# Optimization experiments

Measured on AMD Instinct MI355X. Metric: run time of the kernel, lower is better.

Reference implementation:

```python
import jax, jax.numpy as jnp
import numpy as np

P_IN = 32  # MODEL_CONFIG['p_in']; note: all 32 sample points share the same offsets in the source


def _bilinear_border(feat, sx, sy):
    """Replicates F.grid_sample(mode='bilinear', padding_mode='border', align_corners=False)
    for a single point per (b, n). feat: [B,C,H,W]; sx, sy: [B,N] in pixel coords.
    align_corners=False unnormalization of grid built as 2*s/size - 1 gives px = s - 0.5.
    Returns [B,N,C]."""
    H, W = feat.shape[-2], feat.shape[-1]
    px = jnp.clip(sx - 0.5, 0.0, W - 1.0)  # border padding clamps coords
    py = jnp.clip(sy - 0.5, 0.0, H - 1.0)
    x0 = jnp.floor(px)
    y0 = jnp.floor(py)
    wx = (px - x0)[..., None]  # [B,N,1]
    wy = (py - y0)[..., None]
    x0i = x0.astype(jnp.int32)
    y0i = y0.astype(jnp.int32)
    x1i = jnp.minimum(x0i + 1, W - 1)
    y1i = jnp.minimum(y0i + 1, H - 1)

    def gather(f, yi, xi):  # f [C,H,W], yi/xi [N] -> [N,C]
        return f[:, yi, xi].T

    g = jax.vmap(gather)  # over batch
    v00 = g(feat, y0i, x0i)
    v01 = g(feat, y0i, x1i)
    v10 = g(feat, y1i, x0i)
    v11 = g(feat, y1i, x1i)
    return (v00 * (1 - wx) * (1 - wy) + v01 * wx * (1 - wy)
            + v10 * (1 - wx) * wy + v11 * wx * wy)


def _forward(feats, query_pos, query_content, W_off, b_off, sigma_z):
    offsets = query_content @ W_off + b_off  # [B,N,3]
    x, y, z, r = (query_pos[..., i] for i in range(4))
    dx, dy, dz = offsets[..., 0], offsets[..., 1], offsets[..., 2]
    sx = x + dx * (2.0 ** (z - r))
    sy = y + dy * (2.0 ** (z + r))
    sz = z + dz
    L = len(feats)
    levels = jnp.arange(L, dtype=sz.dtype)
    # gaussian z weight, then softmax over levels (as in source: softmax of the exp values)
    w = jnp.exp(-((sz[..., None] - levels) ** 2) / (2.0 * sigma_z ** 2))  # [B,N,L]
    zw = jax.nn.softmax(w, axis=-1)
    out = sum(zw[..., l:l + 1] * _bilinear_border(feats[l], sx, sy) for l in range(L))  # [B,N,C]
    B, N, C = out.shape
    # all P_IN sample points use identical coords in the source -> broadcast
    return jnp.broadcast_to(out[:, :, None, :], (B, N, P_IN, C))


def setup_inputs() -> dict:
    key = jax.random.key(0)
    ks = jax.random.split(key, 8)
    B, N, C = 8, 300, 256
    sizes = [(100, 100), (50, 50), (25, 25), (13, 13)]
    feats = [jax.random.normal(ks[i], (B, C, h, w), dtype=jnp.float32)
             for i, (h, w) in enumerate(sizes)]
    u = jax.random.uniform(ks[4], (B, N, 4), dtype=jnp.float32)
    # x in [0,100), y in [0,100) (level-0 pixel coords), z in [0,4), r in [0,1)
    query_pos = u * jnp.array([100.0, 100.0, 4.0, 1.0], dtype=jnp.float32)
    query_content = jax.random.normal(ks[5], (B, N, C), dtype=jnp.float32)
    W_off = jax.random.normal(ks[6], (C, 3), dtype=jnp.float32) * 0.02
    b_off = jnp.zeros((3,), dtype=jnp.float32)
    sigma_z = jnp.ones((1,), dtype=jnp.float32) * 0.5
    return {"feat0": feats[0], "feat1": feats[1], "feat2": feats[2], "feat3": feats[3],
            "query_pos": query_pos, "query_content": query_content,
            "W_off": W_off, "b_off": b_off, "sigma_z": sigma_z}


def reference(feat0, feat1, feat2, feat3, query_pos, query_content, W_off, b_off, sigma_z):
    return _forward([feat0, feat1, feat2, feat3], query_pos, query_content, W_off, b_off, sigma_z)
```

## Files before the change

kernel.cpp:

```cpp
#include <hip/hip_runtime.h>

constexpr int Bc = 8;
constexpr int Nc = 300;
constexpr int Cc = 256;
constexpr int Pc = 32;

typedef float f32x4 __attribute__((ext_vector_type(4)));

constexpr int L1_OFF = 0;
constexpr int L2_OFF = 2500;
constexpr int L3_OFF = 3125;
constexpr int STAGE_FLOATS = 3296;

__device__ __forceinline__ void gl_lds16(const void* g, void* l) {
    __builtin_amdgcn_global_load_lds(
        (const __attribute__((address_space(1))) void*)g,
        (__attribute__((address_space(3))) void*)l, 16, 0, 0);
}
__device__ __forceinline__ void gl_lds4(const void* g, void* l) {
    __builtin_amdgcn_global_load_lds(
        (const __attribute__((address_space(1))) void*)g,
        (__attribute__((address_space(3))) void*)l, 4, 0, 0);
}

__global__ __launch_bounds__(256) void params_kernel(
    const float* __restrict__ qpos, const float* __restrict__ qcont,
    const float* __restrict__ Woff, const float* __restrict__ boff,
    const float* __restrict__ sigma, float* __restrict__ params)
{
    const int w = threadIdx.x >> 6;
    const int lane = threadIdx.x & 63;
    const int q = blockIdx.x * 4 + w;

    f32x4 qc = *(const f32x4*)&qcont[(size_t)q * Cc + lane * 4];
    float p0 = 0.f, p1 = 0.f, p2 = 0.f;
#pragma unroll
    for (int j = 0; j < 4; ++j) {
        const float* wr = &Woff[(lane * 4 + j) * 3];
        p0 += qc[j] * wr[0];
        p1 += qc[j] * wr[1];
        p2 += qc[j] * wr[2];
    }
#pragma unroll
    for (int off = 32; off > 0; off >>= 1) {
        p0 += __shfl_down(p0, off, 64);
        p1 += __shfl_down(p1, off, 64);
        p2 += __shfl_down(p2, off, 64);
    }
    if (lane == 0) {
        float dx = p0 + boff[0];
        float dy = p1 + boff[1];
        float dz = p2 + boff[2];
        float x = qpos[q * 4 + 0];
        float y = qpos[q * 4 + 1];
        float z = qpos[q * 4 + 2];
        float r = qpos[q * 4 + 3];
        float sx = x + dx * exp2f(z - r);
        float sy = y + dy * exp2f(z + r);
        float sz = z + dz;
        float sg = sigma[0];
        float inv = 1.0f / (2.0f * sg * sg);
        float e[4];
        float s = 0.f;
#pragma unroll
        for (int l = 0; l < 4; ++l) {
            float d = sz - (float)l;
            float wgt = __expf(-d * d * inv);
            e[l] = __expf(wgt);
            s += e[l];
        }
        float rs = 1.0f / s;
        params[q * 8 + 0] = sx;
        params[q * 8 + 1] = sy;
#pragma unroll
        for (int l = 0; l < 4; ++l) params[q * 8 + 2 + l] = e[l] * rs;
    }
}

struct BilinW { int i00, i01, i10, i11; float wx, wy; };
__device__ __forceinline__ BilinW bilin(int W, float sx, float sy) {
    float px = fminf(fmaxf(sx - 0.5f, 0.f), (float)(W - 1));
    float py = fminf(fmaxf(sy - 0.5f, 0.f), (float)(W - 1));
    float x0f = floorf(px);
    float y0f = floorf(py);
    int x0 = (int)x0f;
    int y0 = (int)y0f;
    int x1 = min(x0 + 1, W - 1);
    int y1 = min(y0 + 1, W - 1);
    BilinW r;
    r.wx = px - x0f;
    r.wy = py - y0f;
    r.i00 = y0 * W + x0; r.i01 = y0 * W + x1;
    r.i10 = y1 * W + x0; r.i11 = y1 * W + x1;
    return r;
}
__device__ __forceinline__ float blend(float v00, float v01, float v10, float v11,
                                       float wx, float wy) {
    float top = v00 + wx * (v01 - v00);
    float bot = v10 + wx * (v11 - v10);
    return top + wy * (bot - top);
}

__global__ __launch_bounds__(256, 8) void sample_kernel(
    const float* __restrict__ f0, const float* __restrict__ f1,
    const float* __restrict__ f2, const float* __restrict__ f3,
    const float* __restrict__ params, float* __restrict__ outT)
{
    __shared__ __align__(16) float sl[STAGE_FLOATS];
    const int bc = blockIdx.x;
    const int t = threadIdx.x;
    const int b = bc >> 8;
    const int wave = t >> 6;
    const int lane = t & 63;

    const int q0 = b * Nc + t;
    const bool has2 = (t < Nc - 256);
    f32x4 pa0 = *(const f32x4*)&params[(size_t)q0 * 8];
    f32x4 pb0 = *(const f32x4*)&params[(size_t)q0 * 8 + 4];
    f32x4 pa1 = {0, 0, 0, 0}, pb1 = {0, 0, 0, 0};
    if (has2) {
        pa1 = *(const f32x4*)&params[(size_t)(q0 + 256) * 8];
        pb1 = *(const f32x4*)&params[(size_t)(q0 + 256) * 8 + 4];
    }
    const float sx0 = pa0.x, sy0 = pa0.y;
    const float sx1 = pa1.x, sy1 = pa1.y;

    {
        const char* g1 = (const char*)(f1 + (size_t)bc * 2500);
        char* l1 = (char*)&sl[L1_OFF];
        for (int i = wave; i < 9; i += 4)
            gl_lds16(g1 + i * 1024 + lane * 16, l1 + i * 1024);
        if (wave == 2 && lane < 49)
            gl_lds16(g1 + 9 * 1024 + lane * 16, l1 + 9 * 1024);
        const char* g2 = (const char*)(f2 + (size_t)bc * 625);
        char* l2 = (char*)&sl[L2_OFF];
        for (int i = wave; i < 9; i += 4)
            gl_lds4(g2 + i * 256 + lane * 4, l2 + i * 256);
        if (wave == 1 && lane < 49)
            gl_lds4(g2 + 9 * 256 + lane * 4, l2 + 9 * 256);
        const char* g3 = (const char*)(f3 + (size_t)bc * 169);
        char* l3 = (char*)&sl[L3_OFF];
        for (int i = wave; i < 2; i += 4)
            gl_lds4(g3 + i * 256 + lane * 4, l3 + i * 256);
        if (wave == 3 && lane < 41)
            gl_lds4(g3 + 2 * 256 + lane * 4, l3 + 2 * 256);
    }

    const float* base0 = f0 + (size_t)bc * 10000;
    const BilinW w00 = bilin(100, sx0, sy0);
    float a00 = base0[w00.i00];
    float a01 = base0[w00.i01];
    float a10 = base0[w00.i10];
    float a11 = base0[w00.i11];
    BilinW w01;
    float b00 = 0.f, b01 = 0.f, b10 = 0.f, b11 = 0.f;
    if (has2) {
        w01 = bilin(100, sx1, sy1);
        b00 = base0[w01.i00];
        b01 = base0[w01.i01];
        b10 = base0[w01.i10];
        b11 = base0[w01.i11];
    }

    __syncthreads();

    {
        BilinW w1 = bilin(50, sx0, sy0);
        BilinW w2 = bilin(25, sx0, sy0);
        BilinW w3 = bilin(13, sx0, sy0);
        float acc = pa0.z * blend(a00, a01, a10, a11, w00.wx, w00.wy)
                  + pa0.w * blend(sl[L1_OFF + w1.i00], sl[L1_OFF + w1.i01],
                                  sl[L1_OFF + w1.i10], sl[L1_OFF + w1.i11], w1.wx, w1.wy)
                  + pb0.x * blend(sl[L2_OFF + w2.i00], sl[L2_OFF + w2.i01],
                                  sl[L2_OFF + w2.i10], sl[L2_OFF + w2.i11], w2.wx, w2.wy)
                  + pb0.y * blend(sl[L3_OFF + w3.i00], sl[L3_OFF + w3.i01],
                                  sl[L3_OFF + w3.i10], sl[L3_OFF + w3.i11], w3.wx, w3.wy);
        outT[(size_t)bc * Nc + t] = acc;
    }
    if (has2) {
        BilinW w1 = bilin(50, sx1, sy1);
        BilinW w2 = bilin(25, sx1, sy1);
        BilinW w3 = bilin(13, sx1, sy1);
        float acc = pa1.z * blend(b00, b01, b10, b11, w01.wx, w01.wy)
                  + pa1.w * blend(sl[L1_OFF + w1.i00], sl[L1_OFF + w1.i01],
                                  sl[L1_OFF + w1.i10], sl[L1_OFF + w1.i11], w1.wx, w1.wy)
                  + pb1.x * blend(sl[L2_OFF + w2.i00], sl[L2_OFF + w2.i01],
                                  sl[L2_OFF + w2.i10], sl[L2_OFF + w2.i11], w2.wx, w2.wy)
                  + pb1.y * blend(sl[L3_OFF + w3.i00], sl[L3_OFF + w3.i01],
                                  sl[L3_OFF + w3.i10], sl[L3_OFF + w3.i11], w3.wx, w3.wy);
        outT[(size_t)bc * Nc + t + 256] = acc;
    }
}

__global__ __launch_bounds__(256) void broadcast_kernel(
    const float* __restrict__ outT, float* __restrict__ out)
{
    __shared__ float sval[Cc];
    const int q = blockIdx.x;
    const int b = q / Nc;
    const int n = q - b * Nc;
    const int c = threadIdx.x;
    sval[c] = outT[((size_t)(b * Cc + c)) * Nc + n];
    __syncthreads();

    const int wave = threadIdx.x >> 6;
    const int c4 = (threadIdx.x & 63) * 4;
    f32x4 val = *(const f32x4*)&sval[c4];
    float* obase = out + (size_t)q * (Pc * Cc) + c4;
#pragma unroll
    for (int p = wave; p < Pc; p += 4) {
        __builtin_nontemporal_store(val, (f32x4*)(obase + p * Cc));
    }
}

__global__ __launch_bounds__(256) void sampling3d_fallback(
    const float* __restrict__ f0, const float* __restrict__ f1,
    const float* __restrict__ f2, const float* __restrict__ f3,
    const float* __restrict__ qpos, const float* __restrict__ qcont,
    const float* __restrict__ Woff, const float* __restrict__ boff,
    const float* __restrict__ sigma, float* __restrict__ out)
{
    const int q = blockIdx.x;
    const int b = q / Nc;
    const int c = threadIdx.x;
    float qc = qcont[q * Cc + c];
    float p0 = qc * Woff[c * 3 + 0];
    float p1 = qc * Woff[c * 3 + 1];
    float p2 = qc * Woff[c * 3 + 2];
#pragma unroll
    for (int off = 32; off > 0; off >>= 1) {
        p0 += __shfl_down(p0, off, 64);
        p1 += __shfl_down(p1, off, 64);
        p2 += __shfl_down(p2, off, 64);
    }
    __shared__ float red[4][3];
    __shared__ float par[8];
    __shared__ float accs[Cc];
    const int wave = threadIdx.x >> 6;
    if ((threadIdx.x & 63) == 0) { red[wave][0] = p0; red[wave][1] = p1; red[wave][2] = p2; }
    __syncthreads();
    if (threadIdx.x == 0) {
        float dx = red[0][0] + red[1][0] + red[2][0] + red[3][0] + boff[0];
        float dy = red[0][1] + red[1][1] + red[2][1] + red[3][1] + boff[1];
        float dz = red[0][2] + red[1][2] + red[2][2] + red[3][2] + boff[2];
        float x = qpos[q * 4 + 0], y = qpos[q * 4 + 1];
        float z = qpos[q * 4 + 2], r = qpos[q * 4 + 3];
        float sx = x + dx * exp2f(z - r);
        float sy = y + dy * exp2f(z + r);
        float sz = z + dz;
        float sg = sigma[0];
        float inv = 1.0f / (2.0f * sg * sg);
        float e[4]; float s = 0.f;
#pragma unroll
        for (int l = 0; l < 4; ++l) {
            float d = sz - (float)l;
            float w = __expf(-d * d * inv);
            e[l] = __expf(w);
            s += e[l];
        }
        float rs = 1.0f / s;
        par[0] = sx; par[1] = sy;
#pragma unroll
        for (int l = 0; l < 4; ++l) par[2 + l] = e[l] * rs;
    }
    __syncthreads();
    const float sx = par[0];
    const float sy = par[1];
    const float* const fs[4] = {f0, f1, f2, f3};
    const int HWs[4] = {100, 50, 25, 13};
    float acc = 0.f;
#pragma unroll
    for (int l = 0; l < 4; ++l) {
        const int W = HWs[l];
        float px = fminf(fmaxf(sx - 0.5f, 0.f), (float)(W - 1));
        float py = fminf(fmaxf(sy - 0.5f, 0.f), (float)(W - 1));
        float x0f = floorf(px), y0f = floorf(py);
        float wx = px - x0f, wy = py - y0f;
        int x0 = (int)x0f, y0 = (int)y0f;
        int x1 = min(x0 + 1, W - 1), y1 = min(y0 + 1, W - 1);
        const float* base = fs[l] + (size_t)((b * Cc + c) * W) * W;
        float v00 = base[y0 * W + x0];
        float v01 = base[y0 * W + x1];
        float v10 = base[y1 * W + x0];
        float v11 = base[y1 * W + x1];
        float top = v00 + wx * (v01 - v00);
        float bot = v10 + wx * (v11 - v10);
        acc += par[2 + l] * (top + wy * (bot - top));
    }
    accs[c] = acc;
    __syncthreads();
    const int c4 = (threadIdx.x & 63) * 4;
    f32x4 val = *(const f32x4*)&accs[c4];
    float* obase = out + (size_t)q * (Pc * Cc) + c4;
#pragma unroll
    for (int p = wave; p < Pc; p += 4) {
        __builtin_nontemporal_store(val, (f32x4*)(obase + p * Cc));
    }
}

extern "C" void kernel_launch(void* const* d_in, const int* in_sizes, int n_in,
                              void* d_out, int out_size, void* d_ws, size_t ws_size,
                              hipStream_t stream) {
    const float* f0    = (const float*)d_in[0];
    const float* f1    = (const float*)d_in[1];
    const float* f2    = (const float*)d_in[2];
    const float* f3    = (const float*)d_in[3];
    const float* qpos  = (const float*)d_in[4];
    const float* qcont = (const float*)d_in[5];
    const float* Woff  = (const float*)d_in[6];
    const float* boff  = (const float*)d_in[7];
    const float* sigma = (const float*)d_in[8];
    float* out = (float*)d_out;

    const size_t params_bytes = (size_t)Bc * Nc * 8 * sizeof(float);
    const size_t outT_bytes   = (size_t)Bc * Cc * Nc * sizeof(float);

    if (ws_size >= params_bytes + outT_bytes) {
        float* params = (float*)d_ws;
        float* outT   = (float*)((char*)d_ws + params_bytes);
        params_kernel<<<Bc * Nc / 4, 256, 0, stream>>>(qpos, qcont, Woff, boff, sigma, params);
        sample_kernel<<<Bc * Cc, 256, 0, stream>>>(f0, f1, f2, f3, params, outT);
        broadcast_kernel<<<Bc * Nc, 256, 0, stream>>>(outT, out);
    } else {
        sampling3d_fallback<<<Bc * Nc, 256, 0, stream>>>(
            f0, f1, f2, f3, qpos, qcont, Woff, boff, sigma, out);
    }
}
```

Before: 187.3 us.

## Stage level-0 feature map in LDS and broadcast four queries per block

The sample kernel now copies the whole 100x100 level-0 channel plane into shared memory with async global-to-LDS loads, replacing scattered per-thread global gathers. LDS use rises to about 53 KB per block, so occupancy is lowered to 3 blocks, and the kernel reads all 40 KB of f0 per channel instead of only the touched pixels. The broadcast kernel now handles four queries per block, using one vector load from outT per thread, and launches a quarter as many blocks.

New measurement: 189.5 us. Within noise of the previous version (+1.2%).

```diff
diff --git a/kernel.cpp b/kernel.cpp
--- a/kernel.cpp
+++ b/kernel.cpp
@@ -7,10 +7,11 @@
 
 typedef float f32x4 __attribute__((ext_vector_type(4)));
 
-constexpr int L1_OFF = 0;
-constexpr int L2_OFF = 2500;
-constexpr int L3_OFF = 3125;
-constexpr int STAGE_FLOATS = 3296;
+constexpr int F0_OFF = 0;
+constexpr int S1_OFF = 10000;
+constexpr int S2_OFF = 12500;
+constexpr int S3_OFF = 13125;
+constexpr int STAGE2_FLOATS = 13296;
 
 __device__ __forceinline__ void gl_lds16(const void* g, void* l) {
     __builtin_amdgcn_global_load_lds(
@@ -101,12 +102,12 @@
     return top + wy * (bot - top);
 }
 
-__global__ __launch_bounds__(256, 8) void sample_kernel(
+__global__ __launch_bounds__(256, 3) void sample_kernel(
     const float* __restrict__ f0, const float* __restrict__ f1,
     const float* __restrict__ f2, const float* __restrict__ f3,
     const float* __restrict__ params, float* __restrict__ outT)
 {
-    __shared__ __align__(16) float sl[STAGE_FLOATS];
+    __shared__ __align__(16) float sl[STAGE2_FLOATS];
     const int bc = blockIdx.x;
     const int t = threadIdx.x;
     const int b = bc >> 8;
@@ -126,68 +127,62 @@
     const float sx1 = pa1.x, sy1 = pa1.y;
 
     {
+        const char* g0 = (const char*)(f0 + (size_t)bc * 10000);
+        char* l0 = (char*)&sl[F0_OFF];
+        for (int i = wave; i < 39; i += 4)
+            gl_lds16(g0 + i * 1024 + lane * 16, l0 + i * 1024);
+        if (wave == 0 && lane < 4)
+            gl_lds16(g0 + 39 * 1024 + lane * 16, l0 + 39 * 1024);
         const char* g1 = (const char*)(f1 + (size_t)bc * 2500);
-        char* l1 = (char*)&sl[L1_OFF];
+        char* l1 = (char*)&sl[S1_OFF];
         for (int i = wave; i < 9; i += 4)
             gl_lds16(g1 + i * 1024 + lane * 16, l1 + i * 1024);
-        if (wave == 2 && lane < 49)
+        if (wave == 1 && lane < 49)
             gl_lds16(g1 + 9 * 1024 + lane * 16, l1 + 9 * 1024);
         const char* g2 = (const char*)(f2 + (size_t)bc * 625);
-        char* l2 = (char*)&sl[L2_OFF];
+        char* l2 = (char*)&sl[S2_OFF];
         for (int i = wave; i < 9; i += 4)
             gl_lds4(g2 + i * 256 + lane * 4, l2 + i * 256);
-        if (wave == 1 && lane < 49)
+        if (wave == 2 && lane < 49)
             gl_lds4(g2 + 9 * 256 + lane * 4, l2 + 9 * 256);
         const char* g3 = (const char*)(f3 + (size_t)bc * 169);
-        char* l3 = (char*)&sl[L3_OFF];
+        char* l3 = (char*)&sl[S3_OFF];
         for (int i = wave; i < 2; i += 4)
             gl_lds4(g3 + i * 256 + lane * 4, l3 + i * 256);
         if (wave == 3 && lane < 41)
             gl_lds4(g3 + 2 * 256 + lane * 4, l3 + 2 * 256);
     }
 
-    const float* base0 = f0 + (size_t)bc * 10000;
-    const BilinW w00 = bilin(100, sx0, sy0);
-    float a00 = base0[w00.i00];
-    float a01 = base0[w00.i01];
-    float a10 = base0[w00.i10];
-    float a11 = base0[w00.i11];
-    BilinW w01;
-    float b00 = 0.f, b01 = 0.f, b10 = 0.f, b11 = 0.f;
-    if (has2) {
-        w01 = bilin(100, sx1, sy1);
-        b00 = base0[w01.i00];
-        b01 = base0[w01.i01];
-        b10 = base0[w01.i10];
-        b11 = base0[w01.i11];
-    }
-
     __syncthreads();
 
     {
+        BilinW w0 = bilin(100, sx0, sy0);
         BilinW w1 = bilin(50, sx0, sy0);
         BilinW w2 = bilin(25, sx0, sy0);
         BilinW w3 = bilin(13, sx0, sy0);
-        float acc = pa0.z * blend(a00, a01, a10, a11, w00.wx, w00.wy)
-                  + pa0.w * blend(sl[L1_OFF + w1.i00], sl[L1_OFF + w1.i01],
-                                  sl[L1_OFF + w1.i10], sl[L1_OFF + w1.i11], w1.wx, w1.wy)
-                  + pb0.x * blend(sl[L2_OFF + w2.i00], sl[L2_OFF + w2.i01],
-                                  sl[L2_OFF + w2.i10], sl[L2_OFF + w2.i11], w2.wx, w2.wy)
-                  + pb0.y * blend(sl[L3_OFF + w3.i00], sl[L3_OFF + w3.i01],
-                                  sl[L3_OFF + w3.i10], sl[L3_OFF + w3.i11], w3.wx, w3.wy);
+        float acc = pa0.z * blend(sl[F0_OFF + w0.i00], sl[F0_OFF + w0.i01],
+                                  sl[F0_OFF + w0.i10], sl[F0_OFF + w0.i11], w0.wx, w0.wy)
+                  + pa0.w * blend(sl[S1_OFF + w1.i00], sl[S1_OFF + w1.i01],
+                                  sl[S1_OFF + w1.i10], sl[S1_OFF + w1.i11], w1.wx, w1.wy)
+                  + pb0.x * blend(sl[S2_OFF + w2.i00], sl[S2_OFF + w2.i01],
+                                  sl[S2_OFF + w2.i10], sl[S2_OFF + w2.i11], w2.wx, w2.wy)
+                  + pb0.y * blend(sl[S3_OFF + w3.i00], sl[S3_OFF + w3.i01],
+                                  sl[S3_OFF + w3.i10], sl[S3_OFF + w3.i11], w3.wx, w3.wy);
         outT[(size_t)bc * Nc + t] = acc;
     }
     if (has2) {
+        BilinW w0 = bilin(100, sx1, sy1);
         BilinW w1 = bilin(50, sx1, sy1);
         BilinW w2 = bilin(25, sx1, sy1);
         BilinW w3 = bilin(13, sx1, sy1);
-        float acc = pa1.z * blend(b00, b01, b10, b11, w01.wx, w01.wy)
-                  + pa1.w * blend(sl[L1_OFF + w1.i00], sl[L1_OFF + w1.i01],
-                                  sl[L1_OFF + w1.i10], sl[L1_OFF + w1.i11], w1.wx, w1.wy)
-                  + pb1.x * blend(sl[L2_OFF + w2.i00], sl[L2_OFF + w2.i01],
-                                  sl[L2_OFF + w2.i10], sl[L2_OFF + w2.i11], w2.wx, w2.wy)
-                  + pb1.y * blend(sl[L3_OFF + w3.i00], sl[L3_OFF + w3.i01],
-                                  sl[L3_OFF + w3.i10], sl[L3_OFF + w3.i11], w3.wx, w3.wy);
+        float acc = pa1.z * blend(sl[F0_OFF + w0.i00], sl[F0_OFF + w0.i01],
+                                  sl[F0_OFF + w0.i10], sl[F0_OFF + w0.i11], w0.wx, w0.wy)
+                  + pa1.w * blend(sl[S1_OFF + w1.i00], sl[S1_OFF + w1.i01],
+                                  sl[S1_OFF + w1.i10], sl[S1_OFF + w1.i11], w1.wx, w1.wy)
+                  + pb1.x * blend(sl[S2_OFF + w2.i00], sl[S2_OFF + w2.i01],
+                                  sl[S2_OFF + w2.i10], sl[S2_OFF + w2.i11], w2.wx, w2.wy)
+                  + pb1.y * blend(sl[S3_OFF + w3.i00], sl[S3_OFF + w3.i01],
+                                  sl[S3_OFF + w3.i10], sl[S3_OFF + w3.i11], w3.wx, w3.wy);
         outT[(size_t)bc * Nc + t + 256] = acc;
     }
 }
@@ -195,21 +190,26 @@
 __global__ __launch_bounds__(256) void broadcast_kernel(
     const float* __restrict__ outT, float* __restrict__ out)
 {
-    __shared__ float sval[Cc];
-    const int q = blockIdx.x;
-    const int b = q / Nc;
-    const int n = q - b * Nc;
+    __shared__ float sval[4][Cc];
+    const int q0 = blockIdx.x * 4;
+    const int b = q0 / Nc;
+    const int n0 = q0 - b * Nc;
     const int c = threadIdx.x;
-    sval[c] = outT[((size_t)(b * Cc + c)) * Nc + n];
+    f32x4 v = *(const f32x4*)&outT[((size_t)(b * Cc + c)) * Nc + n0];
+#pragma unroll
+    for (int j = 0; j < 4; ++j) sval[j][c] = v[j];
     __syncthreads();
 
     const int wave = threadIdx.x >> 6;
     const int c4 = (threadIdx.x & 63) * 4;
-    f32x4 val = *(const f32x4*)&sval[c4];
-    float* obase = out + (size_t)q * (Pc * Cc) + c4;
-#pragma unroll
-    for (int p = wave; p < Pc; p += 4) {
-        __builtin_nontemporal_store(val, (f32x4*)(obase + p * Cc));
+#pragma unroll
+    for (int j = 0; j < 4; ++j) {
+        f32x4 val = *(const f32x4*)&sval[j][c4];
+        float* obase = out + (size_t)(q0 + j) * (Pc * Cc) + c4;
+#pragma unroll
+        for (int p = wave; p < Pc; p += 4) {
+            __builtin_nontemporal_store(val, (f32x4*)(obase + p * Cc));
+        }
     }
 }
 
@@ -320,7 +320,7 @@
         float* outT   = (float*)((char*)d_ws + params_bytes);
         params_kernel<<<Bc * Nc / 4, 256, 0, stream>>>(qpos, qcont, Woff, boff, sigma, params);
         sample_kernel<<<Bc * Cc, 256, 0, stream>>>(f0, f1, f2, f3, params, outT);
-        broadcast_kernel<<<Bc * Nc, 256, 0, stream>>>(outT, out);
+        broadcast_kernel<<<Bc * Nc / 4, 256, 0, stream>>>(outT, out);
     } else {
         sampling3d_fallback<<<Bc * Nc, 256, 0, stream>>>(
             f0, f1, f2, f3, qpos, qcont, Woff, boff, sigma, out);
```
